# Performance work log

Hardware: AMD Instinct MI355X
Metric: run time of the kernel (lower is better)

Reference implementation:

```python
import jax, jax.numpy as jnp
import numpy as np

N_NODES = 50000


def gcn_conv(x, W, b, row, col, n):
    """PyG GCNConv with default add_self_loops=True, normalize=True.
    out[i] = sum_{e: col[e]=i} d^-1/2[row[e]] d^-1/2[i] * (x@W)[row[e]]
             + d^-1[i]*(x@W)[i] + b,  where d = in-degree + 1 (self-loop).
    """
    x_lin = x @ W                                   # [n, out_ch]
    ones = jnp.ones(row.shape[0], dtype=x.dtype)
    deg = jax.ops.segment_sum(ones, col, num_segments=n) + 1.0  # self-loop
    dinv = jax.lax.rsqrt(deg)                       # deg >= 1, safe
    norm = dinv[row] * dinv[col]                    # [E]
    msg = norm[:, None] * x_lin[row]                # [E, out_ch]
    agg = jax.ops.segment_sum(msg, col, num_segments=n)
    self_term = (dinv * dinv)[:, None] * x_lin      # self-loop contribution
    return agg + self_term + b


def setup_inputs() -> dict:
    key = jax.random.key(0)
    ks = jax.random.split(key, 10)
    in_ch, hid, out_ch = 128, 256, 64
    E = 800000
    x = jax.random.normal(ks[0], (N_NODES, in_ch), dtype=jnp.float32)
    edge_attr = jax.random.normal(ks[1], (E, 8), dtype=jnp.float32)  # unused by forward
    edge_index = jax.random.randint(ks[2], (2, E), 0, N_NODES, dtype=jnp.int64)
    def glorot(k, fan_in, fan_out):
        s = float(np.sqrt(6.0 / (fan_in + fan_out)))
        return jax.random.uniform(k, (fan_in, fan_out), jnp.float32, -s, s)
    return {
        "x": x,
        "edge_attr": edge_attr,
        "edge_index": edge_index,
        "W1": glorot(ks[3], in_ch, hid), "b1": jnp.zeros((hid,), jnp.float32),
        "W2": glorot(ks[4], hid, hid),  "b2": jnp.zeros((hid,), jnp.float32),
        "W3": glorot(ks[5], hid, out_ch), "b3": jnp.zeros((out_ch,), jnp.float32),
    }


def reference(x, edge_attr, edge_index, W1, b1, W2, b2, W3, b3):
    n = x.shape[0]
    row, col = edge_index[0], edge_index[1]
    h = jax.nn.sigmoid(gcn_conv(x, W1, b1, row, col, n))
    h = jax.nn.sigmoid(gcn_conv(h, W2, b2, row, col, n))
    # dropout(p=0.1) in eval mode is identity
    return gcn_conv(h, W3, b3, row, col, n)
```

## Files before the change

### kernel.cpp

```cpp
#include <hip/hip_runtime.h>
#include <hip/hip_bf16.h>

typedef __bf16 bf16x8_t __attribute__((ext_vector_type(8)));
typedef float f32x4_t __attribute__((ext_vector_type(4)));

__device__ __forceinline__ float bits2f(unsigned int u) {
    union { unsigned int u; float f; } c; c.u = u; return c.f;
}
__device__ __forceinline__ unsigned short f2bf_bits(float f) {
    __hip_bfloat16 h = __float2bfloat16(f);
    return __builtin_bit_cast(unsigned short, h);
}

__global__ void sentinel_fill(float* __restrict__ out, int n) {
    int i = blockIdx.x * blockDim.x + threadIdx.x;
    if (i < n) out[i] = 100.0f;
}

__global__ void detect_ei(const unsigned int* __restrict__ ei, int* __restrict__ flags) {
    int lane = threadIdx.x;
    int cz = 0;
    #pragma unroll
    for (int j = 0; j < 4; ++j) {
        int idx = lane * 4 + j;
        cz += (ei[2 * idx + 1] == 0u);
    }
    #pragma unroll
    for (int off = 32; off; off >>= 1) cz += __shfl_down(cz, off);
    if (lane == 0) flags[0] = (cz > 200);
}


__global__ void count_edges_dual(const int* __restrict__ ei, int* __restrict__ cnt,
                                 int E, int M, const int* __restrict__ flags) {
    int e = blockIdx.x * blockDim.x + threadIdx.x;
    if (e < E) {
        int c = flags[0] ? ei[2 * E + 2 * e] : ei[E + e];
        if ((unsigned)c < (unsigned)M) atomicAdd(&cnt[c], 1);
    }
}

__global__ void scan_blocks(const int* __restrict__ cnt, int* __restrict__ excl,
                            int* __restrict__ bsum, int n) {
    int tid = threadIdx.x;
    int i = blockIdx.x * 256 + tid;
    int lane = tid & 63, wv = tid >> 6;
    __shared__ int ws[4];
    int v = (i < n) ? cnt[i] : 0;
    int s = v;
    #pragma unroll
    for (int off = 1; off < 64; off <<= 1) {
        int t = __shfl_up(s, off);
        if (lane >= off) s += t;
    }
    if (lane == 63) ws[wv] = s;
    __syncthreads();
    if (tid == 0) { int a = 0; for (int q = 0; q < 4; ++q) { int t = ws[q]; ws[q] = a; a += t; } }
    __syncthreads();
    int ex = s - v + ws[wv];
    if (i < n) excl[i] = ex;
    if (tid == 255) bsum[blockIdx.x] = ex + v;
}

__global__ void scan_bsums(const int* __restrict__ bsum, int* __restrict__ boff,
                           int nb, int* __restrict__ colptr, int n) {
    int tid = threadIdx.x, lane = tid & 63, wv = tid >> 6;
    __shared__ int ws[4];
    __shared__ int carry;
    if (tid == 0) carry = 0;
    __syncthreads();
    for (int base = 0; base < nb; base += 256) {
        int i = base + tid;
        int v = (i < nb) ? bsum[i] : 0;
        int s = v;
        #pragma unroll
        for (int off = 1; off < 64; off <<= 1) {
            int t = __shfl_up(s, off);
            if (lane >= off) s += t;
        }
        if (lane == 63) ws[wv] = s;
        __syncthreads();
        if (tid == 0) { int a = carry; for (int q = 0; q < 4; ++q) { int t = ws[q]; ws[q] = a; a += t; } carry = a; }
        __syncthreads();
        int ex = s - v + ws[wv];
        if (i < nb) boff[i] = ex;
        __syncthreads();
    }
    if (tid == 0) colptr[n] = carry;
}

__global__ void scan_add_dinv(const int* __restrict__ excl, const int* __restrict__ boff,
                              const int* __restrict__ cnt, int* __restrict__ colptr,
                              int* __restrict__ cursor, float* __restrict__ dinv, int n) {
    int i = blockIdx.x * 256 + threadIdx.x;
    if (i < n) {
        int v = excl[i] + boff[blockIdx.x];
        colptr[i] = v;
        cursor[i] = v;
        dinv[i] = rsqrtf((float)cnt[i] + 1.0f);
    }
}

__global__ void fill_csr_dual(const int* __restrict__ ei, int* __restrict__ cursor,
                              int* __restrict__ esrc, int E, int M,
                              const int* __restrict__ flags) {
    int e = blockIdx.x * blockDim.x + threadIdx.x;
    if (e < E) {
        int r, c;
        if (flags[0]) { r = ei[2 * e]; c = ei[2 * E + 2 * e]; }
        else          { r = ei[e];     c = ei[E + e]; }
        if ((unsigned)c < (unsigned)M && (unsigned)r < (unsigned)M) {
            int p = atomicAdd(&cursor[c], 1);
            if ((unsigned)p < (unsigned)E) esrc[p] = r;
        }
    }
}

__global__ void transpose_all(const float* __restrict__ W1, const float* __restrict__ W2,
                              const float* __restrict__ W3,
                              unsigned short* __restrict__ Wt1, unsigned short* __restrict__ Wt2,
                              unsigned short* __restrict__ Wt3) {
    int i = blockIdx.x * 256 + threadIdx.x;
    if (i < 32768) {
        int k = i >> 8, n = i & 255;
        Wt1[n * 128 + k] = f2bf_bits(W1[i]);
    } else if (i < 32768 + 65536) {
        int j = i - 32768;
        int k = j >> 8, n = j & 255;
        Wt2[n * 256 + k] = f2bf_bits(W2[j]);
    } else if (i < 114688) {
        int j = i - 98304;
        int k = j >> 6, n = j & 63;
        Wt3[n * 256 + k] = f2bf_bits(W3[j]);
    }
}

__global__ void prescale_x(const float* __restrict__ x, const float* __restrict__ dinv,
                           unsigned short* __restrict__ xs, int total) {
    int i = blockIdx.x * 256 + threadIdx.x;
    if (i < total) {
        int row = i >> 7;
        xs[i] = f2bf_bits(x[i] * dinv[row]);
    }
}

template<int K, int BN, int NTOT, int EPI>
__global__ __launch_bounds__(256) void gemm_tile(
    const __bf16* __restrict__ A,
    const unsigned short* __restrict__ Bt,
    const float* __restrict__ dinv,
    const float* __restrict__ bias,
    void* __restrict__ Y,
    int M)
{
    constexpr int KS = (K > 128) ? 128 : K;
    constexpr int KP = KS + 8;
    constexpr int NT = BN / 2 / 16;
    __shared__ unsigned short Bs[BN * KP];

    const int tid  = threadIdx.x;
    const int lane = tid & 63;
    const int wave = tid >> 6;
    const int wm   = wave >> 1;
    const int wn   = wave & 1;
    const int quad = lane >> 4;
    const int l16  = lane & 15;
    const int n0   = blockIdx.y * BN;

    int mrow[4];
#pragma unroll
    for (int mt = 0; mt < 4; ++mt) {
        int r = blockIdx.x * 128 + wm * 64 + mt * 16 + l16;
        mrow[mt] = (r < M) ? r : (M - 1);
    }

    f32x4_t acc[4][NT];
#pragma unroll
    for (int mt = 0; mt < 4; ++mt)
#pragma unroll
        for (int t = 0; t < NT; ++t) acc[mt][t] = (f32x4_t){0.f, 0.f, 0.f, 0.f};

    const unsigned short* BsW = &Bs[(wn * (BN / 2)) * KP];

    for (int kh = 0; kh < K; kh += KS) {
        constexpr int CH = BN * KS / 8;
        for (int idx = tid; idx < CH; idx += 256) {
            int n  = idx / (KS / 8);
            int k8 = idx - n * (KS / 8);
            uint4 v = *(const uint4*)(Bt + (size_t)(n0 + n) * K + kh + k8 * 8);
            *(uint4*)&Bs[n * KP + k8 * 8] = v;
        }
        __syncthreads();

#pragma unroll
        for (int kc = 0; kc < KS; kc += 32) {
            bf16x8_t a[4], b[NT];
#pragma unroll
            for (int mt = 0; mt < 4; ++mt)
                a[mt] = *(const bf16x8_t*)(A + (size_t)mrow[mt] * K + kh + kc + quad * 8);
#pragma unroll
            for (int t = 0; t < NT; ++t)
                b[t] = *(const bf16x8_t*)&BsW[(t * 16 + l16) * KP + kc + quad * 8];
#pragma unroll
            for (int mt = 0; mt < 4; ++mt)
#pragma unroll
                for (int t = 0; t < NT; ++t)
                    acc[mt][t] = __builtin_amdgcn_mfma_f32_16x16x32_bf16(a[mt], b[t], acc[mt][t], 0, 0, 0);
        }
        if (kh + KS < K) __syncthreads();
    }

    float bv[NT];
    if constexpr (EPI == 1) {
#pragma unroll
        for (int t = 0; t < NT; ++t)
            bv[t] = bias[n0 + wn * (BN / 2) + t * 16 + l16];
    }

#pragma unroll
    for (int mt = 0; mt < 4; ++mt) {
        int rowbase = blockIdx.x * 128 + wm * 64 + mt * 16 + quad * 4;
#pragma unroll
        for (int r = 0; r < 4; ++r) {
            int rrow = rowbase + r;
            if (rrow < M) {
                if constexpr (EPI == 0) {
                    float dv = dinv[rrow];
#pragma unroll
                    for (int t = 0; t < NT; ++t) {
                        int ccol = n0 + wn * (BN / 2) + t * 16 + l16;
                        ((__hip_bfloat16*)Y)[(size_t)rrow * NTOT + ccol] =
                            __float2bfloat16(acc[mt][t][r] * dv);
                    }
                } else if constexpr (EPI == 1) {
#pragma unroll
                    for (int t = 0; t < NT; ++t) {
                        int ccol = n0 + wn * (BN / 2) + t * 16 + l16;
                        float o = acc[mt][t][r] + bv[t];
                        o = 1.f / (1.f + __expf(-o));
                        ((__hip_bfloat16*)Y)[(size_t)rrow * NTOT + ccol] = __float2bfloat16(o);
                    }
                } else {
                    float dv = dinv[rrow];
#pragma unroll
                    for (int t = 0; t < NT; ++t) {
                        int ccol = n0 + wn * (BN / 2) + t * 16 + l16;
                        float o = acc[mt][t][r] * dv;
                        int pk = __builtin_amdgcn_cvt_pk_fp8_f32(o, o, 0, false);
                        ((unsigned char*)Y)[(size_t)rrow * NTOT + ccol] = (unsigned char)(pk & 0xff);
                    }
                }
            }
        }
    }
}

__global__ __launch_bounds__(256) void aggregate_fp8_256(
    const unsigned char* __restrict__ Y8,
    const int* __restrict__ colptr,
    const int* __restrict__ esrc,
    const float* __restrict__ dinv,
    const float* __restrict__ bias,
    unsigned short* __restrict__ H,
    int M, int Etot)
{
    const int lane = threadIdx.x & 63;
    const int wave = threadIdx.x >> 6;
    const int l = lane & 15;
    const int g = lane >> 4;
    int node = blockIdx.x * 4 + wave;
    if (node >= M) return;

    int s = colptr[node];
    int e = colptr[node + 1];
    if (s < 0) s = 0;
    if (e > Etot) e = Etot;
    if (e < s) e = s;

    const char* Yb = (const char*)Y8;
    const unsigned loff = (unsigned)(l * 16);

    float acc[16];
    #pragma unroll
    for (int k = 0; k < 16; ++k) acc[k] = 0.f;

    auto unpack = [&](uint4 u) {
        auto p0 = __builtin_amdgcn_cvt_pk_f32_fp8(u.x, false);
        auto p1 = __builtin_amdgcn_cvt_pk_f32_fp8(u.x, true);
        auto p2 = __builtin_amdgcn_cvt_pk_f32_fp8(u.y, false);
        auto p3 = __builtin_amdgcn_cvt_pk_f32_fp8(u.y, true);
        auto p4 = __builtin_amdgcn_cvt_pk_f32_fp8(u.z, false);
        auto p5 = __builtin_amdgcn_cvt_pk_f32_fp8(u.z, true);
        auto p6 = __builtin_amdgcn_cvt_pk_f32_fp8(u.w, false);
        auto p7 = __builtin_amdgcn_cvt_pk_f32_fp8(u.w, true);
        acc[0]  += p0[0]; acc[1]  += p0[1];
        acc[2]  += p1[0]; acc[3]  += p1[1];
        acc[4]  += p2[0]; acc[5]  += p2[1];
        acc[6]  += p3[0]; acc[7]  += p3[1];
        acc[8]  += p4[0]; acc[9]  += p4[1];
        acc[10] += p5[0]; acc[11] += p5[1];
        acc[12] += p6[0]; acc[13] += p6[1];
        acc[14] += p7[0]; acc[15] += p7[1];
    };

    for (int base = s; base < e; base += 64) {
        int n = e - base; if (n > 64) n = 64;
        unsigned myOff = 0;
        if (lane < n) myOff = (unsigned)esrc[base + lane] << 8;
        int j = 0;
        #pragma unroll 2
        for (; j + 4 <= n; j += 4) {
            unsigned off = __shfl(myOff, j + g) + loff;
            uint4 u = *(const uint4*)(Yb + off);
            unpack(u);
        }
        if (j < n) {
            unsigned off = __shfl(myOff, j + g) + loff;
            if (j + g < n) {
                uint4 u = *(const uint4*)(Yb + off);
                unpack(u);
            }
        }
    }
    if (g == 0) {
        uint4 u = *(const uint4*)(Yb + ((unsigned)node << 8) + loff);
        unpack(u);
    }
    #pragma unroll
    for (int off = 16; off < 64; off <<= 1) {
        #pragma unroll
        for (int k = 0; k < 16; ++k) acc[k] += __shfl_xor(acc[k], off);
    }

    if (g == 0) {
        float dv = dinv[node];
        float o[16];
        #pragma unroll
        for (int k = 0; k < 16; ++k) {
            o[k] = acc[k] * dv + bias[l * 16 + k];
            o[k] = 1.f / (1.f + __expf(-o[k]));
        }
        uint4 s0, s1;
        s0.x = (unsigned)f2bf_bits(o[0])  | ((unsigned)f2bf_bits(o[1])  << 16);
        s0.y = (unsigned)f2bf_bits(o[2])  | ((unsigned)f2bf_bits(o[3])  << 16);
        s0.z = (unsigned)f2bf_bits(o[4])  | ((unsigned)f2bf_bits(o[5])  << 16);
        s0.w = (unsigned)f2bf_bits(o[6])  | ((unsigned)f2bf_bits(o[7])  << 16);
        s1.x = (unsigned)f2bf_bits(o[8])  | ((unsigned)f2bf_bits(o[9])  << 16);
        s1.y = (unsigned)f2bf_bits(o[10]) | ((unsigned)f2bf_bits(o[11]) << 16);
        s1.z = (unsigned)f2bf_bits(o[12]) | ((unsigned)f2bf_bits(o[13]) << 16);
        s1.w = (unsigned)f2bf_bits(o[14]) | ((unsigned)f2bf_bits(o[15]) << 16);
        unsigned short* Hp = H + (size_t)node * 256 + l * 16;
        *(uint4*)Hp       = s0;
        *(uint4*)(Hp + 8) = s1;
    }
}

template<int C, bool SIG, bool OUTF32, bool HASB>
__global__ __launch_bounds__(256) void aggregate2(
    const unsigned short* __restrict__ Y,
    const int* __restrict__ colptr,
    const int* __restrict__ esrc,
    const float* __restrict__ dinv,
    const float* __restrict__ bias,
    void* __restrict__ H,
    int M, int Etot)
{
    constexpr int G   = C / 8;
    constexpr int EPW = 64 / G;
    const int lane = threadIdx.x & 63;
    const int wave = threadIdx.x >> 6;
    const int l = lane & (G - 1);
    const int g = lane / G;
    int node = blockIdx.x * 4 + wave;
    if (node >= M) return;

    int s = colptr[node];
    int e = colptr[node + 1];
    if (s < 0) s = 0;
    if (e > Etot) e = Etot;
    if (e < s) e = s;

    const char* Yb = (const char*)Y;
    const unsigned loff = (unsigned)(l * 16);

    float acc[8];
    #pragma unroll
    for (int k = 0; k < 8; ++k) acc[k] = 0.f;

    auto unpack = [&](uint4 u) {
        acc[0] += bits2f(u.x << 16);
        acc[1] += bits2f(u.x & 0xffff0000u);
        acc[2] += bits2f(u.y << 16);
        acc[3] += bits2f(u.y & 0xffff0000u);
        acc[4] += bits2f(u.z << 16);
        acc[5] += bits2f(u.z & 0xffff0000u);
        acc[6] += bits2f(u.w << 16);
        acc[7] += bits2f(u.w & 0xffff0000u);
    };

    for (int base = s; base < e; base += 64) {
        int n = e - base; if (n > 64) n = 64;
        unsigned myOff = 0;
        if (lane < n) myOff = (unsigned)esrc[base + lane] * (unsigned)(C * 2);
        int j = 0;
        #pragma unroll 2
        for (; j + EPW <= n; j += EPW) {
            unsigned off = __shfl(myOff, j + g) + loff;
            uint4 u = *(const uint4*)(Yb + off);
            unpack(u);
        }
        if (j < n) {
            unsigned off = __shfl(myOff, j + g) + loff;
            if (j + g < n) {
                uint4 u = *(const uint4*)(Yb + off);
                unpack(u);
            }
        }
    }
    if (g == 0) {
        unsigned off = (unsigned)node * (unsigned)(C * 2) + loff;
        uint4 u = *(const uint4*)(Yb + off);
        unpack(u);
    }
    #pragma unroll
    for (int off = G; off < 64; off <<= 1) {
        #pragma unroll
        for (int k = 0; k < 8; ++k) acc[k] += __shfl_xor(acc[k], off);
    }

    if (g == 0) {
        float dv = dinv[node];
        float o[8];
        #pragma unroll
        for (int k = 0; k < 8; ++k) {
            o[k] = acc[k] * dv;
            if (HASB) o[k] += bias[l * 8 + k];
            if (SIG) o[k] = 1.f / (1.f + __expf(-o[k]));
        }
        if constexpr (OUTF32) {
            float* Hp = (float*)H + (size_t)node * C + l * 8;
            *(float4*)Hp       = (float4){o[0], o[1], o[2], o[3]};
            *(float4*)(Hp + 4) = (float4){o[4], o[5], o[6], o[7]};
        } else {
            uint4 st;
            st.x = (unsigned)f2bf_bits(o[0]) | ((unsigned)f2bf_bits(o[1]) << 16);
            st.y = (unsigned)f2bf_bits(o[2]) | ((unsigned)f2bf_bits(o[3]) << 16);
            st.z = (unsigned)f2bf_bits(o[4]) | ((unsigned)f2bf_bits(o[5]) << 16);
            st.w = (unsigned)f2bf_bits(o[6]) | ((unsigned)f2bf_bits(o[7]) << 16);
            *(uint4*)((unsigned short*)H + (size_t)node * C + l * 8) = st;
        }
    }
}


extern "C" void kernel_launch(void* const* d_in, const int* in_sizes, int n_in,
                              void* d_out, int out_size, void* d_ws, size_t ws_size,
                              hipStream_t stream)
{
    int iEI = 2, iW1 = 3, iB1 = 4, iW2 = 5, iB2 = 6, iW3 = 7, iB3 = 8;
    if (n_in == 8) { iEI = 1; iW1 = 2; iB1 = 3; iW2 = 4; iB2 = 5; iW3 = 6; iB3 = 7; }

    const float* x  = (const float*)d_in[0];
    const int* ei   = (const int*)d_in[iEI];
    const float* W1 = (const float*)d_in[iW1];
    const float* b1 = (const float*)d_in[iB1];
    const float* W2 = (const float*)d_in[iW2];
    const float* b2 = (const float*)d_in[iB2];
    const float* W3 = (const float*)d_in[iW3];
    const float* b3 = (const float*)d_in[iB3];

    const int M = in_sizes[0] / 128;
    const int E = in_sizes[iEI] / 2;
    const int NB = (M + 255) / 256;

    auto rnd = [](size_t b) { return (b + 255) & ~(size_t)255; };
    size_t needed = rnd(64 * 4)
                  + rnd((size_t)M * 4) * 2
                  + rnd((size_t)(M + 1) * 4)
                  + rnd((size_t)M * 4)
                  + rnd((size_t)M * 4)
                  + rnd((size_t)(NB + 1) * 4) * 2
                  + rnd((size_t)E * 4)
                  + rnd((size_t)256 * 128 * 2)
                  + rnd((size_t)256 * 256 * 2)
                  + rnd((size_t)64 * 256 * 2)
                  + rnd((size_t)M * 256 * 2) * 2;
    if (ws_size < needed) {
        sentinel_fill<<<(out_size + 255) / 256, 256, 0, stream>>>((float*)d_out, out_size);
        return;
    }

    char* p = (char*)d_ws;
    auto alloc = [&](size_t bytes) {
        char* r = p;
        p += (bytes + 255) & ~(size_t)255;
        return r;
    };
    int* flags  = (int*)alloc(64 * 4);
    float* dinv = (float*)alloc((size_t)M * 4);
    int* cnt    = (int*)alloc((size_t)M * 4);
    int* colptr = (int*)alloc((size_t)(M + 1) * 4);
    int* cursor = (int*)alloc((size_t)M * 4);
    int* excl   = (int*)alloc((size_t)M * 4);
    int* bsum   = (int*)alloc((size_t)(NB + 1) * 4);
    int* boff   = (int*)alloc((size_t)(NB + 1) * 4);
    int* esrc   = (int*)alloc((size_t)E * 4);
    unsigned short* Wt1 = (unsigned short*)alloc((size_t)256 * 128 * 2);
    unsigned short* Wt2 = (unsigned short*)alloc((size_t)256 * 256 * 2);
    unsigned short* Wt3 = (unsigned short*)alloc((size_t)64 * 256 * 2);
    __hip_bfloat16* ybuf = (__hip_bfloat16*)alloc((size_t)M * 256 * 2);
    __hip_bfloat16* hbuf = (__hip_bfloat16*)alloc((size_t)M * 256 * 2);

    unsigned short* xs = (unsigned short*)ybuf;
    unsigned short* xa = (unsigned short*)ybuf + (size_t)M * 128;
    unsigned char*  y8 = (unsigned char*)ybuf;

    detect_ei<<<1, 64, 0, stream>>>((const unsigned int*)ei, flags);

    hipMemsetAsync(cnt, 0, (size_t)M * 4, stream);
    count_edges_dual<<<(E + 255) / 256, 256, 0, stream>>>(ei, cnt, E, M, flags);
    scan_blocks<<<NB, 256, 0, stream>>>(cnt, excl, bsum, M);
    scan_bsums<<<1, 256, 0, stream>>>(bsum, boff, NB, colptr, M);
    scan_add_dinv<<<NB, 256, 0, stream>>>(excl, boff, cnt, colptr, cursor, dinv, M);
    fill_csr_dual<<<(E + 255) / 256, 256, 0, stream>>>(ei, cursor, esrc, E, M, flags);
    transpose_all<<<(114688 + 255) / 256, 256, 0, stream>>>(W1, W2, W3, Wt1, Wt2, Wt3);

    int gmb = (M + 127) / 128;
    int ga  = (M + 3) / 4;

    prescale_x<<<((M * 128) + 255) / 256, 256, 0, stream>>>(x, dinv, xs, M * 128);
    aggregate2<128, false, false, false><<<ga, 256, 0, stream>>>(
        xs, colptr, esrc, dinv, nullptr, xa, M, E);
    gemm_tile<128, 128, 256, 1><<<dim3(gmb, 2), 256, 0, stream>>>(
        (const __bf16*)xa, Wt1, dinv, b1, hbuf, M);
    gemm_tile<256, 128, 256, 2><<<dim3(gmb, 2), 256, 0, stream>>>(
        (const __bf16*)hbuf, Wt2, dinv, b2, y8, M);
    aggregate_fp8_256<<<ga, 256, 0, stream>>>(
        y8, colptr, esrc, dinv, b2, (unsigned short*)hbuf, M, E);
    gemm_tile<256, 64, 64, 0><<<dim3(gmb, 1), 256, 0, stream>>>(
        (const __bf16*)hbuf, Wt3, dinv, b3, ybuf, M);
    aggregate2<64, false, true, true><<<ga, 256, 0, stream>>>(
        (const unsigned short*)ybuf, colptr, esrc, dinv, b3, d_out, M, E);
}
```

Measured before the change: 382.4 us.

## Record per-edge rank during counting and fill CSR without second atomic pass

The degree-counting kernel now stores each edge's atomicAdd return value as its rank within its destination bucket. The CSR fill then computes the slot as colptr[c] + rank[e] instead of doing a second atomicAdd on a cursor array. The fill is also split into 8 destination-range partitions, each block handling one partition, to localize scattered writes. The cost is an extra E-sized rank array plus 8x redundant reads of edge_index and rank in the fill kernel.

```diff
diff --git a/kernel.cpp b/kernel.cpp
--- a/kernel.cpp
+++ b/kernel.cpp
@@ -31,12 +31,15 @@
 }
 
 
-__global__ void count_edges_dual(const int* __restrict__ ei, int* __restrict__ cnt,
-                                 int E, int M, const int* __restrict__ flags) {
+__global__ void count_rank_dual(const int* __restrict__ ei, int* __restrict__ cnt,
+                                int* __restrict__ rank, int E, int M,
+                                const int* __restrict__ flags) {
     int e = blockIdx.x * blockDim.x + threadIdx.x;
     if (e < E) {
         int c = flags[0] ? ei[2 * E + 2 * e] : ei[E + e];
-        if ((unsigned)c < (unsigned)M) atomicAdd(&cnt[c], 1);
+        int rk = 0;
+        if ((unsigned)c < (unsigned)M) rk = atomicAdd(&cnt[c], 1);
+        rank[e] = rk;
     }
 }
 
@@ -91,26 +94,27 @@
 
 __global__ void scan_add_dinv(const int* __restrict__ excl, const int* __restrict__ boff,
                               const int* __restrict__ cnt, int* __restrict__ colptr,
-                              int* __restrict__ cursor, float* __restrict__ dinv, int n) {
+                              float* __restrict__ dinv, int n) {
     int i = blockIdx.x * 256 + threadIdx.x;
     if (i < n) {
-        int v = excl[i] + boff[blockIdx.x];
-        colptr[i] = v;
-        cursor[i] = v;
+        colptr[i] = excl[i] + boff[blockIdx.x];
         dinv[i] = rsqrtf((float)cnt[i] + 1.0f);
     }
 }
 
-__global__ void fill_csr_dual(const int* __restrict__ ei, int* __restrict__ cursor,
-                              int* __restrict__ esrc, int E, int M,
-                              const int* __restrict__ flags) {
-    int e = blockIdx.x * blockDim.x + threadIdx.x;
+__global__ void fill_csr_part(const int* __restrict__ ei, const int* __restrict__ colptr,
+                              const int* __restrict__ rank, int* __restrict__ esrc,
+                              int E, int M, int psz, const int* __restrict__ flags) {
+    int part = blockIdx.x & 7;
+    int e = (blockIdx.x >> 3) * 256 + threadIdx.x;
+    int lo = part * psz;
+    int hi = lo + psz; if (hi > M) hi = M;
     if (e < E) {
         int r, c;
         if (flags[0]) { r = ei[2 * e]; c = ei[2 * E + 2 * e]; }
         else          { r = ei[e];     c = ei[E + e]; }
-        if ((unsigned)c < (unsigned)M && (unsigned)r < (unsigned)M) {
-            int p = atomicAdd(&cursor[c], 1);
+        if (c >= lo && c < hi && (unsigned)r < (unsigned)M) {
+            int p = colptr[c] + rank[e];
             if ((unsigned)p < (unsigned)E) esrc[p] = r;
         }
     }
@@ -472,15 +476,15 @@
     const int M = in_sizes[0] / 128;
     const int E = in_sizes[iEI] / 2;
     const int NB = (M + 255) / 256;
+    const int PSZ = (M + 7) / 8;
 
     auto rnd = [](size_t b) { return (b + 255) & ~(size_t)255; };
     size_t needed = rnd(64 * 4)
                   + rnd((size_t)M * 4) * 2
                   + rnd((size_t)(M + 1) * 4)
                   + rnd((size_t)M * 4)
-                  + rnd((size_t)M * 4)
                   + rnd((size_t)(NB + 1) * 4) * 2
-                  + rnd((size_t)E * 4)
+                  + rnd((size_t)E * 4) * 2
                   + rnd((size_t)256 * 128 * 2)
                   + rnd((size_t)256 * 256 * 2)
                   + rnd((size_t)64 * 256 * 2)
@@ -500,11 +504,11 @@
     float* dinv = (float*)alloc((size_t)M * 4);
     int* cnt    = (int*)alloc((size_t)M * 4);
     int* colptr = (int*)alloc((size_t)(M + 1) * 4);
-    int* cursor = (int*)alloc((size_t)M * 4);
     int* excl   = (int*)alloc((size_t)M * 4);
     int* bsum   = (int*)alloc((size_t)(NB + 1) * 4);
     int* boff   = (int*)alloc((size_t)(NB + 1) * 4);
     int* esrc   = (int*)alloc((size_t)E * 4);
+    int* rank   = (int*)alloc((size_t)E * 4);
     unsigned short* Wt1 = (unsigned short*)alloc((size_t)256 * 128 * 2);
     unsigned short* Wt2 = (unsigned short*)alloc((size_t)256 * 256 * 2);
     unsigned short* Wt3 = (unsigned short*)alloc((size_t)64 * 256 * 2);
@@ -518,11 +522,12 @@
     detect_ei<<<1, 64, 0, stream>>>((const unsigned int*)ei, flags);
 
     hipMemsetAsync(cnt, 0, (size_t)M * 4, stream);
-    count_edges_dual<<<(E + 255) / 256, 256, 0, stream>>>(ei, cnt, E, M, flags);
+    count_rank_dual<<<(E + 255) / 256, 256, 0, stream>>>(ei, cnt, rank, E, M, flags);
     scan_blocks<<<NB, 256, 0, stream>>>(cnt, excl, bsum, M);
     scan_bsums<<<1, 256, 0, stream>>>(bsum, boff, NB, colptr, M);
-    scan_add_dinv<<<NB, 256, 0, stream>>>(excl, boff, cnt, colptr, cursor, dinv, M);
-    fill_csr_dual<<<(E + 255) / 256, 256, 0, stream>>>(ei, cursor, esrc, E, M, flags);
+    scan_add_dinv<<<NB, 256, 0, stream>>>(excl, boff, cnt, colptr, dinv, M);
+    fill_csr_part<<<((E + 255) / 256) * 8, 256, 0, stream>>>(
+        ei, colptr, rank, esrc, E, M, PSZ, flags);
     transpose_all<<<(114688 + 255) / 256, 256, 0, stream>>>(W1, W2, W3, Wt1, Wt2, Wt3);
 
     int gmb = (M + 127) / 128;
```

Measured after the change: 346.2 us. 9.5% less time.
